# Kernel optimization log

Hardware: AMD Instinct MI355X
Metric: run time of the kernel (lower is better)

## Reference

```python
import jax, jax.numpy as jnp
import numpy as np


def conv1x1(x, w, b):
    # x: [B,C,H,W], w: [O,C], b: [O]
    return jnp.einsum('oc,bchw->bohw', w, x) + b[None, :, None, None]


def interp_bilinear_ac(x, oh, ow):
    # bilinear resize with align_corners=True, x: [B,C,H,W] -> [B,C,oh,ow]
    B, C, H, W = x.shape
    if (H, W) == (oh, ow):
        return x
    ys = jnp.linspace(0.0, H - 1.0, oh)
    xs = jnp.linspace(0.0, W - 1.0, ow)
    y0 = jnp.clip(jnp.floor(ys).astype(jnp.int32), 0, H - 1)
    y1 = jnp.minimum(y0 + 1, H - 1)
    x0 = jnp.clip(jnp.floor(xs).astype(jnp.int32), 0, W - 1)
    x1 = jnp.minimum(x0 + 1, W - 1)
    wy = (ys - y0).astype(x.dtype)
    wx = (xs - x0).astype(x.dtype)
    top = x[:, :, y0, :] * (1 - wy)[None, None, :, None] + x[:, :, y1, :] * wy[None, None, :, None]
    out = top[:, :, :, x0] * (1 - wx)[None, None, None, :] + top[:, :, :, x1] * wx[None, None, None, :]
    return out


def non_local(x, qw, qb, kw, kb, vw, vb, ow_, ob):
    B, C, H, W = x.shape
    HW = H * W
    q = conv1x1(x, qw, qb).reshape(B, -1, HW)  # [B, Ci, HW]
    k = conv1x1(x, kw, kb).reshape(B, -1, HW)
    v = conv1x1(x, vw, vb).reshape(B, -1, HW)
    attn = jnp.einsum('bci,bcj->bij', q, k)     # [B, HW, HW]
    attn = jax.nn.softmax(attn, axis=-1)
    out = jnp.einsum('bcj,bij->bci', v, attn)   # [B, Ci, HW]
    out = out.reshape(B, -1, H, W)
    return conv1x1(out, ow_, ob)


def _forward(x1, x2, x3, x4, qw, qb, kw, kb, vw, vb, ow_, ob, g1w, g1b, g2w, g2b):
    H1, W1 = x1.shape[2], x1.shape[3]
    x2_up = interp_bilinear_ac(x2, H1, W1)
    x3_up = interp_bilinear_ac(x3, H1, W1)
    x4_up = interp_bilinear_ac(x4, H1, W1)
    gf = jnp.concatenate([x1, x2_up, x3_up, x4_up], axis=1)  # [B, 128, H1, W1]
    gf = non_local(gf, qw, qb, kw, kb, vw, vb, ow_, ob)
    h = jax.nn.relu(conv1x1(gf, g1w, g1b))
    sw = jax.nn.sigmoid(conv1x1(h, g2w, g2b))                # [B, 128, H1, W1]
    w1, w2, w3, w4 = sw[:, :32], sw[:, 32:64], sw[:, 64:96], sw[:, 96:128]
    x1_out = x1 * (1 + w1)
    x2_out = x2 * (1 + interp_bilinear_ac(w2, x2.shape[2], x2.shape[3]))
    x3_out = x3 * (1 + interp_bilinear_ac(w3, x3.shape[2], x3.shape[3]))
    x4_out = x4 * (1 + interp_bilinear_ac(w4, x4.shape[2], x4.shape[3]))
    return (x1_out, x2_out, x3_out, x4_out)


def setup_inputs() -> dict:
    key = jax.random.key(0)
    ks = jax.random.split(key, 16)
    C = 128  # channel*4
    Ci = 64  # inter_channel
    Cg = 32
    d = {
        'x1': jax.random.normal(ks[0], (8, 32, 64, 64), jnp.float32),
        'x2': jax.random.normal(ks[1], (8, 32, 32, 32), jnp.float32),
        'x3': jax.random.normal(ks[2], (8, 32, 16, 16), jnp.float32),
        'x4': jax.random.normal(ks[3], (8, 32, 8, 8), jnp.float32),
        'qw': jax.random.normal(ks[4], (Ci, C), jnp.float32) * 0.05,
        'qb': jnp.zeros((Ci,), jnp.float32),
        'kw': jax.random.normal(ks[5], (Ci, C), jnp.float32) * 0.05,
        'kb': jnp.zeros((Ci,), jnp.float32),
        'vw': jax.random.normal(ks[6], (Ci, C), jnp.float32) * 0.05,
        'vb': jnp.zeros((Ci,), jnp.float32),
        'ow_': jax.random.normal(ks[7], (C, Ci), jnp.float32) * 0.05,
        'ob': jnp.zeros((C,), jnp.float32),
        'g1w': jax.random.normal(ks[8], (Cg, C), jnp.float32) * 0.05,
        'g1b': jnp.zeros((Cg,), jnp.float32),
        'g2w': jax.random.normal(ks[9], (C, Cg), jnp.float32) * 0.05,
        'g2b': jnp.zeros((C,), jnp.float32),
    }
    return d


def reference(x1, x2, x3, x4, qw, qb, kw, kb, vw, vb, ow_, ob, g1w, g1b, g2w, g2b):
    return _forward(x1, x2, x3, x4, qw, qb, kw, kb, vw, vb, ow_, ob, g1w, g1b, g2w, g2b)
```

## Files before the change

kernel.cpp:

```cpp
#include <hip/hip_runtime.h>
#include <hip/hip_bf16.h>


typedef __attribute__((ext_vector_type(8))) short s16x8;
typedef __attribute__((ext_vector_type(4))) float f32x4;

#define LOG2E 1.44269504088896340736f

__device__ __forceinline__ unsigned int f2bf(float f) {
    unsigned int u = __float_as_uint(f);
    u += 0x7fffu + ((u >> 16) & 1u);
    return u >> 16;
}
__device__ __forceinline__ unsigned int pk2bf(float a, float b) {
    union { __hip_bfloat162 h; unsigned int u; } cv;
    cv.h = __float22bfloat162_rn(make_float2(a, b));
    return cv.u;
}
__device__ __forceinline__ float bf2f(unsigned short u) {
    return __uint_as_float((unsigned int)u << 16);
}

__global__ __launch_bounds__(256) void k_prep(
    const float* __restrict__ qw, const float* __restrict__ qb,
    const float* __restrict__ kw, const float* __restrict__ kb,
    const float* __restrict__ vw, const float* __restrict__ vb,
    const float* __restrict__ ow, const float* __restrict__ g1w,
    const float* __restrict__ g2w,
    unsigned short* __restrict__ WTb, float* __restrict__ bqkv,
    unsigned short* __restrict__ owb, unsigned short* __restrict__ g1wb,
    unsigned short* __restrict__ g2wb) {
  int t = blockIdx.x * 256 + threadIdx.x;
  if (t < 192 * 128) {
    int oc = t >> 7, c = t & 127;
    float v;
    if (oc < 64)       v = qw[oc * 128 + c] * LOG2E;
    else if (oc < 128) v = kw[(oc - 64) * 128 + c];
    else               v = vw[(oc - 128) * 128 + c];
    WTb[t] = (unsigned short)f2bf(v);
  }
  if (t < 192) {
    float v;
    if (t < 64)       v = qb[t] * LOG2E;
    else if (t < 128) v = kb[t - 64];
    else              v = vb[t - 128];
    bqkv[t] = v;
  }
  if (t < 128 * 64) g1wb[t & 4095] = (unsigned short)f2bf(g1w[t & 4095]);
  if (t < 128 * 64) owb[t] = (unsigned short)f2bf(ow[t]);
  if (t < 128 * 32) g2wb[t] = (unsigned short)f2bf(g2w[t]);
}

__global__ __launch_bounds__(256) void k_qkv(
    const float* __restrict__ x1, const float* __restrict__ x2,
    const float* __restrict__ x3, const float* __restrict__ x4,
    const unsigned short* __restrict__ WTb, const float* __restrict__ bqkv,
    unsigned short* __restrict__ Qg, unsigned short* __restrict__ Kg,
    unsigned short* __restrict__ Vg) {
  __shared__ __align__(16) unsigned short gfb[128 * 136];
  unsigned int* gfbu = (unsigned int*)gfb;

  const int b = blockIdx.x >> 5;
  const int i0 = (blockIdx.x & 31) << 7;
  const int t = threadIdx.x;

  {
    const int cp = t >> 2, q = t & 3;
    const int c0 = cp << 1;
    const int pbase = q << 5;
    const int oy = (i0 >> 6) + (q >> 1);
    const int ox0 = (q & 1) << 5;

    if (cp < 16) {
      const float* s0 = x1 + (((b * 32 + c0) << 12) + (oy << 6) + ox0);
      const float* s1 = s0 + 4096;
      #pragma unroll
      for (int k8 = 0; k8 < 8; k8++) {
        float4 va = ((const float4*)s0)[k8];
        float4 vb = ((const float4*)s1)[k8];
        int p = pbase + k8 * 4;
        gfbu[(p + 0) * 68 + cp] = pk2bf(va.x, vb.x);
        gfbu[(p + 1) * 68 + cp] = pk2bf(va.y, vb.y);
        gfbu[(p + 2) * 68 + cp] = pk2bf(va.z, vb.z);
        gfbu[(p + 3) * 68 + cp] = pk2bf(va.w, vb.w);
      }
    } else {
      const float* base; int S, cs;
      if (cp < 32)      { base = x2; S = 32; cs = c0 - 32; }
      else if (cp < 48) { base = x3; S = 16; cs = c0 - 64; }
      else              { base = x4; S = 8;  cs = c0 - 96; }
      const float* pl0 = base + (b * 32 + cs) * S * S;
      const float* pl1 = pl0 + S * S;
      float yf = (float)oy * (float)(S - 1) * (1.0f / 63.0f);
      int y0 = (int)yf; if (y0 > S - 1) y0 = S - 1;
      int y1 = y0 + 1;  if (y1 > S - 1) y1 = S - 1;
      float wy = yf - (float)y0;
      const float* r00 = pl0 + y0 * S; const float* r01 = pl0 + y1 * S;
      const float* r10 = pl1 + y0 * S; const float* r11 = pl1 + y1 * S;
      for (int k = 0; k < 32; k++) {
        int ox = ox0 + k;
        float xf = (float)ox * (float)(S - 1) * (1.0f / 63.0f);
        int xx0 = (int)xf; if (xx0 > S - 1) xx0 = S - 1;
        int xx1 = xx0 + 1; if (xx1 > S - 1) xx1 = S - 1;
        float wx = xf - (float)xx0;
        float a0 = r00[xx0] + wx * (r00[xx1] - r00[xx0]);
        float b0 = r01[xx0] + wx * (r01[xx1] - r01[xx0]);
        float v0 = a0 + wy * (b0 - a0);
        float a1 = r10[xx0] + wx * (r10[xx1] - r10[xx0]);
        float b1 = r11[xx0] + wx * (r11[xx1] - r11[xx0]);
        float v1 = a1 + wy * (b1 - a1);
        gfbu[(pbase + k) * 68 + cp] = pk2bf(v0, v1);
      }
    }
  }
  __syncthreads();

  const int wv = t >> 6, lane = t & 63;
  const int r = lane & 15, qd = lane >> 4;
  const int ocb = wv * 48;

  s16x8 af[3][4];
  #pragma unroll
  for (int mti = 0; mti < 3; mti++)
    #pragma unroll
    for (int ks = 0; ks < 4; ks++)
      af[mti][ks] = *(const s16x8*)&WTb[(ocb + mti * 16 + r) * 128 + ks * 32 + qd * 8];
  float4 bias[3];
  #pragma unroll
  for (int mti = 0; mti < 3; mti++)
    bias[mti] = *(const float4*)&bqkv[ocb + mti * 16 + qd * 4];

  f32x4 zf = {0.f, 0.f, 0.f, 0.f};
  #pragma unroll 1
  for (int nt = 0; nt < 8; nt++) {
    s16x8 bfr[4];
    #pragma unroll
    for (int ks = 0; ks < 4; ks++)
      bfr[ks] = *(const s16x8*)&gfb[(nt * 16 + r) * 136 + ks * 32 + qd * 8];
    f32x4 acc[3] = {zf, zf, zf};
    #pragma unroll
    for (int ks = 0; ks < 4; ks++)
      #pragma unroll
      for (int mti = 0; mti < 3; mti++)
        acc[mti] = __builtin_amdgcn_mfma_f32_16x16x32_bf16(af[mti][ks], bfr[ks], acc[mti], 0, 0, 0);

    const int pos = i0 + nt * 16 + r;
    #pragma unroll
    for (int mti = 0; mti < 3; mti++) {
      const int gmt = wv * 3 + mti;
      float ax = acc[mti].x + bias[mti].x;
      float ay = acc[mti].y + bias[mti].y;
      float az = acc[mti].z + bias[mti].z;
      float aw = acc[mti].w + bias[mti].w;
      if (gmt < 4) {
        uint2 w; w.x = pk2bf(ax, ay); w.y = pk2bf(az, aw);
        *(uint2*)&Qg[(((b << 12) + pos) << 6) + gmt * 16 + qd * 4] = w;
      } else if (gmt < 8) {
        uint2 w; w.x = pk2bf(ax, ay); w.y = pk2bf(az, aw);
        *(uint2*)&Kg[(((b << 12) + pos) << 6) + (gmt - 4) * 16 + qd * 4] = w;
      } else {
        int ocv = (gmt - 8) * 16 + qd * 4;
        Vg[((b * 64 + ocv + 0) << 12) + pos] = (unsigned short)f2bf(ax);
        Vg[((b * 64 + ocv + 1) << 12) + pos] = (unsigned short)f2bf(ay);
        Vg[((b * 64 + ocv + 2) << 12) + pos] = (unsigned short)f2bf(az);
        Vg[((b * 64 + ocv + 3) << 12) + pos] = (unsigned short)f2bf(aw);
      }
    }
  }
}

__global__ __launch_bounds__(256, 4) void k_attn(
    const unsigned short* __restrict__ Qg, const unsigned short* __restrict__ Kg,
    const unsigned short* __restrict__ Vg, unsigned short* __restrict__ Op,
    float* __restrict__ Lp) {
  __shared__ __align__(16) unsigned short Kl[64 * 72];
  __shared__ __align__(16) unsigned short Vl[64 * 72];
  __shared__ __align__(16) unsigned short Pl[4][32 * 72];

  const int b = blockIdx.x >> 7;
  const int part = (blockIdx.x >> 5) & 3;
  const int qg = blockIdx.x & 31;
  const int i0 = qg << 7;
  const int t = threadIdx.x;
  const int wv = t >> 6, lane = t & 63;
  const int r = lane & 15, qd = lane >> 4;
  const int qbase = i0 + wv * 32;

  s16x8 qf[2][2];
  #pragma unroll
  for (int nt = 0; nt < 2; nt++)
    #pragma unroll
    for (int ks = 0; ks < 2; ks++)
      qf[nt][ks] = *(const s16x8*)&Qg[(((b << 12) + qbase + nt * 16 + r) << 6) + ks * 32 + qd * 8];

  f32x4 zf = {0.f, 0.f, 0.f, 0.f};
  f32x4 acc[2][4];
  #pragma unroll
  for (int nt = 0; nt < 2; nt++)
    #pragma unroll
    for (int mt = 0; mt < 4; mt++) acc[nt][mt] = zf;
  float l[2] = {0.f, 0.f};

  const int srow = t >> 3, sseg = t & 7;
  const unsigned short* kt0 = &Kg[(((b << 12) + (part << 10) + srow) << 6) + sseg * 8];
  const unsigned short* vt0 = &Vg[((b * 64 + srow) << 12) + (part << 10) + sseg * 8];
  uint4 pk0 = *(const uint4*)(kt0);
  uint4 pk1 = *(const uint4*)(kt0 + (32 << 6));
  uint4 pv0 = *(const uint4*)(vt0);
  uint4 pv1 = *(const uint4*)(vt0 + (32 << 12));

  for (int it = 0; it < 16; it++) {
    __syncthreads();
    *(uint4*)&Kl[srow * 72 + sseg * 8] = pk0;
    *(uint4*)&Kl[(srow + 32) * 72 + sseg * 8] = pk1;
    *(uint4*)&Vl[srow * 72 + sseg * 8] = pv0;
    *(uint4*)&Vl[(srow + 32) * 72 + sseg * 8] = pv1;
    __syncthreads();
    if (it < 15) {
      int j0 = (it + 1) << 6;
      pk0 = *(const uint4*)(kt0 + (j0 << 6));
      pk1 = *(const uint4*)(kt0 + ((j0 + 32) << 6));
      pv0 = *(const uint4*)(vt0 + j0);
      pv1 = *(const uint4*)(vt0 + (32 << 12) + j0);
    }

    f32x4 st[4][2];
    #pragma unroll
    for (int mt = 0; mt < 4; mt++) {
      s16x8 kf0 = *(const s16x8*)&Kl[(mt * 16 + r) * 72 + qd * 8];
      s16x8 kf1 = *(const s16x8*)&Kl[(mt * 16 + r) * 72 + 32 + qd * 8];
      #pragma unroll
      for (int nt = 0; nt < 2; nt++) {
        f32x4 s = __builtin_amdgcn_mfma_f32_16x16x32_bf16(kf0, qf[nt][0], zf, 0, 0, 0);
        s = __builtin_amdgcn_mfma_f32_16x16x32_bf16(kf1, qf[nt][1], s, 0, 0, 0);
        st[mt][nt] = s;
      }
    }

    #pragma unroll
    for (int nt = 0; nt < 2; nt++) {
      float rs = 0.f;
      #pragma unroll
      for (int mt = 0; mt < 4; mt++) {
        float px = exp2f(fminf(st[mt][nt].x, 80.f));
        float py = exp2f(fminf(st[mt][nt].y, 80.f));
        float pz = exp2f(fminf(st[mt][nt].z, 80.f));
        float pw = exp2f(fminf(st[mt][nt].w, 80.f));
        rs += (px + py) + (pz + pw);
        uint2 w;
        w.x = pk2bf(px, py);
        w.y = pk2bf(pz, pw);
        *(uint2*)&Pl[wv][(nt * 16 + r) * 72 + mt * 16 + qd * 4] = w;
      }
      rs += __shfl_xor(rs, 16);
      rs += __shfl_xor(rs, 32);
      l[nt] += rs;
    }
    __builtin_amdgcn_wave_barrier();

    #pragma unroll
    for (int ks = 0; ks < 2; ks++) {
      s16x8 pf0 = *(const s16x8*)&Pl[wv][(r) * 72 + ks * 32 + qd * 8];
      s16x8 pf1 = *(const s16x8*)&Pl[wv][(16 + r) * 72 + ks * 32 + qd * 8];
      #pragma unroll
      for (int mt = 0; mt < 4; mt++) {
        s16x8 vf = *(const s16x8*)&Vl[(mt * 16 + r) * 72 + ks * 32 + qd * 8];
        acc[0][mt] = __builtin_amdgcn_mfma_f32_16x16x32_bf16(vf, pf0, acc[0][mt], 0, 0, 0);
        acc[1][mt] = __builtin_amdgcn_mfma_f32_16x16x32_bf16(vf, pf1, acc[1][mt], 0, 0, 0);
      }
    }
  }

  #pragma unroll
  for (int nt = 0; nt < 2; nt++) {
    float inv = 1.0f / l[nt];
    int qrow = qbase + nt * 16 + r;
    unsigned short* orow = &Op[(((part * 8 + b) << 12) + qrow) << 6];
    #pragma unroll
    for (int mt = 0; mt < 4; mt++) {
      uint2 w;
      w.x = pk2bf(acc[nt][mt].x * inv, acc[nt][mt].y * inv);
      w.y = pk2bf(acc[nt][mt].z * inv, acc[nt][mt].w * inv);
      *(uint2*)&orow[mt * 16 + qd * 4] = w;
    }
    if (qd == 0) Lp[((part * 8 + b) << 12) + qrow] = l[nt];
  }
}

__global__ __launch_bounds__(256) void k_out(
    const unsigned short* __restrict__ Op, const float* __restrict__ Lp,
    const unsigned short* __restrict__ owb, const float* __restrict__ obias,
    const unsigned short* __restrict__ g1wb, const float* __restrict__ g1b,
    const unsigned short* __restrict__ g2wb, const float* __restrict__ g2b,
    unsigned short* __restrict__ SWb) {
  __shared__ __align__(16) unsigned short Ot[128 * 72];
  __shared__ __align__(16) unsigned short gf2t[128 * 136];
  __shared__ __align__(16) unsigned short ht[128 * 40];
  const int b = blockIdx.x >> 5;
  const int i0 = (blockIdx.x & 31) << 7;
  const int t = threadIdx.x;

  {
    const int pos = t >> 1, half = t & 1;
    const int i = i0 + pos;
    float lp4[4], lsum = 0.f;
    #pragma unroll
    for (int p = 0; p < 4; p++) { lp4[p] = Lp[((p * 8 + b) << 12) + i]; lsum += lp4[p]; }
    float o[32];
    #pragma unroll
    for (int k = 0; k < 32; k++) o[k] = 0.f;
    #pragma unroll
    for (int p = 0; p < 4; p++) {
      float w = lp4[p] / lsum;
      const uint2* prow = (const uint2*)&Op[((((p * 8 + b) << 12) + i) << 6) + half * 32];
      #pragma unroll
      for (int k = 0; k < 8; k++) {
        uint2 u = prow[k];
        o[k * 4 + 0] += w * __uint_as_float(u.x << 16);
        o[k * 4 + 1] += w * __uint_as_float(u.x & 0xFFFF0000u);
        o[k * 4 + 2] += w * __uint_as_float(u.y << 16);
        o[k * 4 + 3] += w * __uint_as_float(u.y & 0xFFFF0000u);
      }
    }
    unsigned int* dst = (unsigned int*)&Ot[pos * 72 + half * 32];
    #pragma unroll
    for (int k = 0; k < 16; k++) dst[k] = pk2bf(o[2 * k], o[2 * k + 1]);
  }
  __syncthreads();

  const int wv = t >> 6, lane = t & 63;
  const int r = lane & 15, qd = lane >> 4;
  f32x4 zf = {0.f, 0.f, 0.f, 0.f};

  {
    const int ocb = wv * 32;
    s16x8 af[2][2];
    #pragma unroll
    for (int mt = 0; mt < 2; mt++)
      #pragma unroll
      for (int ks = 0; ks < 2; ks++)
        af[mt][ks] = *(const s16x8*)&owb[(ocb + mt * 16 + r) * 64 + ks * 32 + qd * 8];
    float4 bias[2];
    #pragma unroll
    for (int mt = 0; mt < 2; mt++)
      bias[mt] = *(const float4*)&obias[ocb + mt * 16 + qd * 4];
    #pragma unroll 1
    for (int nt = 0; nt < 8; nt++) {
      s16x8 bfr[2];
      #pragma unroll
      for (int ks = 0; ks < 2; ks++)
        bfr[ks] = *(const s16x8*)&Ot[(nt * 16 + r) * 72 + ks * 32 + qd * 8];
      f32x4 acc[2] = {zf, zf};
      #pragma unroll
      for (int ks = 0; ks < 2; ks++)
        #pragma unroll
        for (int mt = 0; mt < 2; mt++)
          acc[mt] = __builtin_amdgcn_mfma_f32_16x16x32_bf16(af[mt][ks], bfr[ks], acc[mt], 0, 0, 0);
      #pragma unroll
      for (int mt = 0; mt < 2; mt++) {
        uint2 w;
        w.x = pk2bf(acc[mt].x + bias[mt].x, acc[mt].y + bias[mt].y);
        w.y = pk2bf(acc[mt].z + bias[mt].z, acc[mt].w + bias[mt].w);
        *(uint2*)&gf2t[(nt * 16 + r) * 136 + ocb + mt * 16 + qd * 4] = w;
      }
    }
  }
  __syncthreads();

  {
    s16x8 af[2][4];
    #pragma unroll
    for (int mt = 0; mt < 2; mt++)
      #pragma unroll
      for (int ks = 0; ks < 4; ks++)
        af[mt][ks] = *(const s16x8*)&g1wb[(mt * 16 + r) * 128 + ks * 32 + qd * 8];
    float4 bias[2];
    #pragma unroll
    for (int mt = 0; mt < 2; mt++)
      bias[mt] = *(const float4*)&g1b[mt * 16 + qd * 4];
    #pragma unroll
    for (int nt = 0; nt < 2; nt++) {
      const int pn = (wv * 2 + nt) * 16 + r;
      s16x8 bfr[4];
      #pragma unroll
      for (int ks = 0; ks < 4; ks++)
        bfr[ks] = *(const s16x8*)&gf2t[pn * 136 + ks * 32 + qd * 8];
      f32x4 acc[2] = {zf, zf};
      #pragma unroll
      for (int ks = 0; ks < 4; ks++)
        #pragma unroll
        for (int mt = 0; mt < 2; mt++)
          acc[mt] = __builtin_amdgcn_mfma_f32_16x16x32_bf16(af[mt][ks], bfr[ks], acc[mt], 0, 0, 0);
      #pragma unroll
      for (int mt = 0; mt < 2; mt++) {
        uint2 w;
        w.x = pk2bf(fmaxf(acc[mt].x + bias[mt].x, 0.f), fmaxf(acc[mt].y + bias[mt].y, 0.f));
        w.y = pk2bf(fmaxf(acc[mt].z + bias[mt].z, 0.f), fmaxf(acc[mt].w + bias[mt].w, 0.f));
        *(uint2*)&ht[pn * 40 + mt * 16 + qd * 4] = w;
      }
    }
  }
  __syncthreads();

  {
    const int nb = wv * 32;
    s16x8 bfg[2];
    float bias[2];
    #pragma unroll
    for (int ntl = 0; ntl < 2; ntl++) {
      bfg[ntl] = *(const s16x8*)&g2wb[(nb + ntl * 16 + r) * 32 + qd * 8];
      bias[ntl] = g2b[nb + ntl * 16 + r];
    }
    #pragma unroll 1
    for (int mt = 0; mt < 8; mt++) {
      s16x8 af = *(const s16x8*)&ht[(mt * 16 + r) * 40 + qd * 8];
      #pragma unroll
      for (int ntl = 0; ntl < 2; ntl++) {
        f32x4 acc = __builtin_amdgcn_mfma_f32_16x16x32_bf16(af, bfg[ntl], zf, 0, 0, 0);
        const int oc3 = nb + ntl * 16 + r;
        float s0 = 1.0f / (1.0f + exp2f(-LOG2E * (acc.x + bias[ntl])));
        float s1 = 1.0f / (1.0f + exp2f(-LOG2E * (acc.y + bias[ntl])));
        float s2 = 1.0f / (1.0f + exp2f(-LOG2E * (acc.z + bias[ntl])));
        float s3 = 1.0f / (1.0f + exp2f(-LOG2E * (acc.w + bias[ntl])));
        uint2 w; w.x = pk2bf(s0, s1); w.y = pk2bf(s2, s3);
        *(uint2*)&SWb[((b * 128 + oc3) << 12) + i0 + mt * 16 + qd * 4] = w;
      }
    }
  }
}

__device__ __forceinline__ float bilin64(const unsigned short* __restrict__ p,
                                         int oy, int ox, int n) {
  float yf = (float)oy * 63.0f / (float)n;
  int y0 = (int)yf; if (y0 > 63) y0 = 63;
  int y1 = y0 + 1;  if (y1 > 63) y1 = 63;
  float wy = yf - (float)y0;
  float xf = (float)ox * 63.0f / (float)n;
  int x0 = (int)xf; if (x0 > 63) x0 = 63;
  int x1 = x0 + 1;  if (x1 > 63) x1 = 63;
  float wx = xf - (float)x0;
  float v00 = bf2f(p[y0 * 64 + x0]), v01 = bf2f(p[y0 * 64 + x1]);
  float v10 = bf2f(p[y1 * 64 + x0]), v11 = bf2f(p[y1 * 64 + x1]);
  float top = v00 + wx * (v01 - v00);
  float bot = v10 + wx * (v11 - v10);
  return top + wy * (bot - top);
}

__global__ __launch_bounds__(256) void k_final(
    const float* __restrict__ x1, const float* __restrict__ x2,
    const float* __restrict__ x3, const float* __restrict__ x4,
    const unsigned short* __restrict__ SWb, float* __restrict__ out) {
  const int N1 = 1048576, N2 = 262144, N3 = 65536, N4 = 16384;
  int idx = blockIdx.x * 256 + threadIdx.x;
  if (idx < N1) {
    int b = idx >> 17, rr = idx & 131071;
    int c = rr >> 12, hw = rr & 4095;
    out[idx] = x1[idx] * (1.f + bf2f(SWb[((b * 128 + c) << 12) + hw]));
  } else if (idx < N1 + N2) {
    int i2 = idx - N1;
    int b = i2 >> 15, rr = i2 & 32767;
    int c = rr >> 10, oy = (rr >> 5) & 31, ox = rr & 31;
    float w = bilin64(SWb + ((b * 128 + 32 + c) << 12), oy, ox, 31);
    out[idx] = x2[i2] * (1.f + w);
  } else if (idx < N1 + N2 + N3) {
    int i3 = idx - N1 - N2;
    int b = i3 >> 13, rr = i3 & 8191;
    int c = rr >> 8, oy = (rr >> 4) & 15, ox = rr & 15;
    float w = bilin64(SWb + ((b * 128 + 64 + c) << 12), oy, ox, 15);
    out[idx] = x3[i3] * (1.f + w);
  } else if (idx < N1 + N2 + N3 + N4) {
    int i4 = idx - N1 - N2 - N3;
    int b = i4 >> 11, rr = i4 & 2047;
    int c = rr >> 6, oy = (rr >> 3) & 7, ox = rr & 7;
    float w = bilin64(SWb + ((b * 128 + 96 + c) << 12), oy, ox, 7);
    out[idx] = x4[i4] * (1.f + w);
  }
}

extern "C" void kernel_launch(void* const* d_in, const int* in_sizes, int n_in,
                              void* d_out, int out_size, void* d_ws, size_t ws_size,
                              hipStream_t stream) {
  const float* x1  = (const float*)d_in[0];
  const float* x2  = (const float*)d_in[1];
  const float* x3  = (const float*)d_in[2];
  const float* x4  = (const float*)d_in[3];
  const float* qw  = (const float*)d_in[4];
  const float* qb  = (const float*)d_in[5];
  const float* kw  = (const float*)d_in[6];
  const float* kb  = (const float*)d_in[7];
  const float* vw  = (const float*)d_in[8];
  const float* vb  = (const float*)d_in[9];
  const float* ow  = (const float*)d_in[10];
  const float* ob  = (const float*)d_in[11];
  const float* g1w = (const float*)d_in[12];
  const float* g1b = (const float*)d_in[13];
  const float* g2w = (const float*)d_in[14];
  const float* g2b = (const float*)d_in[15];
  float* out = (float*)d_out;

  char* ws = (char*)d_ws;
  unsigned short* Qg  = (unsigned short*)(ws + 0);
  unsigned short* Kg  = (unsigned short*)(ws + 4194304);
  unsigned short* Vg  = (unsigned short*)(ws + 8388608);
  unsigned short* SWb = (unsigned short*)(ws + 0);
  unsigned short* Op  = (unsigned short*)(ws + 12582912);
  float* Lp   = (float*)(ws + 29360128);
  unsigned short* WTb = (unsigned short*)(ws + 29884416);
  float* bqkv = (float*)(ws + 29933568);
  unsigned short* owb  = (unsigned short*)(ws + 29934592);
  unsigned short* g1wb = (unsigned short*)(ws + 29950976);
  unsigned short* g2wb = (unsigned short*)(ws + 29959168);

  k_prep<<<96, 256, 0, stream>>>(qw, qb, kw, kb, vw, vb, ow, g1w, g2w,
                                 WTb, bqkv, owb, g1wb, g2wb);
  k_qkv<<<256, 256, 0, stream>>>(x1, x2, x3, x4, WTb, bqkv, Qg, Kg, Vg);
  k_attn<<<1024, 256, 0, stream>>>(Qg, Kg, Vg, Op, Lp);
  k_out<<<256, 256, 0, stream>>>(Op, Lp, owb, ob, g1wb, g1b, g2wb, g2b, SWb);
  k_final<<<5440, 256, 0, stream>>>(x1, x2, x3, x4, SWb, out);
}
```

Before: 201.7 us.

## Compute softmax row sums via MFMA, use fast exp2/rcp, and split qkv tiles

The attention kernel no longer accumulates row sums with per-element adds and cross-lane shuffles. It gets them from an extra MFMA against a ones vector, which also lets exp be fused right after the QK MFMA without a staging array. exp2f and divisions are replaced with hardware exp2/rcp intrinsics in attention, merge and sigmoid, at slightly lower accuracy. k_qkv now processes 64 positions per block with twice as many blocks, halving shared memory to raise occupancy and parallelism.

```diff
diff --git a/kernel.cpp b/kernel.cpp
--- a/kernel.cpp
+++ b/kernel.cpp
@@ -19,6 +19,12 @@
 }
 __device__ __forceinline__ float bf2f(unsigned short u) {
     return __uint_as_float((unsigned int)u << 16);
+}
+__device__ __forceinline__ float fexp2(float x) {
+    return __builtin_amdgcn_exp2f(x);
+}
+__device__ __forceinline__ float frcp(float x) {
+    return __builtin_amdgcn_rcpf(x);
 }
 
 __global__ __launch_bounds__(256) void k_prep(
@@ -57,28 +63,28 @@
     const unsigned short* __restrict__ WTb, const float* __restrict__ bqkv,
     unsigned short* __restrict__ Qg, unsigned short* __restrict__ Kg,
     unsigned short* __restrict__ Vg) {
-  __shared__ __align__(16) unsigned short gfb[128 * 136];
+  __shared__ __align__(16) unsigned short gfb[64 * 136];
   unsigned int* gfbu = (unsigned int*)gfb;
 
-  const int b = blockIdx.x >> 5;
-  const int i0 = (blockIdx.x & 31) << 7;
+  const int b = blockIdx.x >> 6;
+  const int i0 = (blockIdx.x & 63) << 6;
   const int t = threadIdx.x;
 
   {
     const int cp = t >> 2, q = t & 3;
     const int c0 = cp << 1;
-    const int pbase = q << 5;
-    const int oy = (i0 >> 6) + (q >> 1);
-    const int ox0 = (q & 1) << 5;
+    const int pbase = q << 4;
+    const int oy = i0 >> 6;
+    const int ox0 = pbase;
 
     if (cp < 16) {
       const float* s0 = x1 + (((b * 32 + c0) << 12) + (oy << 6) + ox0);
       const float* s1 = s0 + 4096;
       #pragma unroll
-      for (int k8 = 0; k8 < 8; k8++) {
-        float4 va = ((const float4*)s0)[k8];
-        float4 vb = ((const float4*)s1)[k8];
-        int p = pbase + k8 * 4;
+      for (int k4 = 0; k4 < 4; k4++) {
+        float4 va = ((const float4*)s0)[k4];
+        float4 vb = ((const float4*)s1)[k4];
+        int p = pbase + k4 * 4;
         gfbu[(p + 0) * 68 + cp] = pk2bf(va.x, vb.x);
         gfbu[(p + 1) * 68 + cp] = pk2bf(va.y, vb.y);
         gfbu[(p + 2) * 68 + cp] = pk2bf(va.z, vb.z);
@@ -97,7 +103,7 @@
       float wy = yf - (float)y0;
       const float* r00 = pl0 + y0 * S; const float* r01 = pl0 + y1 * S;
       const float* r10 = pl1 + y0 * S; const float* r11 = pl1 + y1 * S;
-      for (int k = 0; k < 32; k++) {
+      for (int k = 0; k < 16; k++) {
         int ox = ox0 + k;
         float xf = (float)ox * (float)(S - 1) * (1.0f / 63.0f);
         int xx0 = (int)xf; if (xx0 > S - 1) xx0 = S - 1;
@@ -132,7 +138,7 @@
 
   f32x4 zf = {0.f, 0.f, 0.f, 0.f};
   #pragma unroll 1
-  for (int nt = 0; nt < 8; nt++) {
+  for (int nt = 0; nt < 4; nt++) {
     s16x8 bfr[4];
     #pragma unroll
     for (int ks = 0; ks < 4; ks++)
@@ -199,7 +205,10 @@
   for (int nt = 0; nt < 2; nt++)
     #pragma unroll
     for (int mt = 0; mt < 4; mt++) acc[nt][mt] = zf;
-  float l[2] = {0.f, 0.f};
+  f32x4 accl[2] = {zf, zf};
+
+  const short ob = (r == 0) ? (short)0x3F80 : (short)0;
+  const s16x8 vones = {ob, ob, ob, ob, ob, ob, ob, ob};
 
   const int srow = t >> 3, sseg = t & 7;
   const unsigned short* kt0 = &Kg[(((b << 12) + (part << 10) + srow) << 6) + sseg * 8];
@@ -224,7 +233,6 @@
       pv1 = *(const uint4*)(vt0 + (32 << 12) + j0);
     }
 
-    f32x4 st[4][2];
     #pragma unroll
     for (int mt = 0; mt < 4; mt++) {
       s16x8 kf0 = *(const s16x8*)&Kl[(mt * 16 + r) * 72 + qd * 8];
@@ -233,28 +241,15 @@
       for (int nt = 0; nt < 2; nt++) {
         f32x4 s = __builtin_amdgcn_mfma_f32_16x16x32_bf16(kf0, qf[nt][0], zf, 0, 0, 0);
         s = __builtin_amdgcn_mfma_f32_16x16x32_bf16(kf1, qf[nt][1], s, 0, 0, 0);
-        st[mt][nt] = s;
-      }
-    }
-
-    #pragma unroll
-    for (int nt = 0; nt < 2; nt++) {
-      float rs = 0.f;
-      #pragma unroll
-      for (int mt = 0; mt < 4; mt++) {
-        float px = exp2f(fminf(st[mt][nt].x, 80.f));
-        float py = exp2f(fminf(st[mt][nt].y, 80.f));
-        float pz = exp2f(fminf(st[mt][nt].z, 80.f));
-        float pw = exp2f(fminf(st[mt][nt].w, 80.f));
-        rs += (px + py) + (pz + pw);
+        float px = fexp2(fminf(s.x, 80.f));
+        float py = fexp2(fminf(s.y, 80.f));
+        float pz = fexp2(fminf(s.z, 80.f));
+        float pw = fexp2(fminf(s.w, 80.f));
         uint2 w;
         w.x = pk2bf(px, py);
         w.y = pk2bf(pz, pw);
         *(uint2*)&Pl[wv][(nt * 16 + r) * 72 + mt * 16 + qd * 4] = w;
       }
-      rs += __shfl_xor(rs, 16);
-      rs += __shfl_xor(rs, 32);
-      l[nt] += rs;
     }
     __builtin_amdgcn_wave_barrier();
 
@@ -268,12 +263,15 @@
         acc[0][mt] = __builtin_amdgcn_mfma_f32_16x16x32_bf16(vf, pf0, acc[0][mt], 0, 0, 0);
         acc[1][mt] = __builtin_amdgcn_mfma_f32_16x16x32_bf16(vf, pf1, acc[1][mt], 0, 0, 0);
       }
+      accl[0] = __builtin_amdgcn_mfma_f32_16x16x32_bf16(vones, pf0, accl[0], 0, 0, 0);
+      accl[1] = __builtin_amdgcn_mfma_f32_16x16x32_bf16(vones, pf1, accl[1], 0, 0, 0);
     }
   }
 
   #pragma unroll
   for (int nt = 0; nt < 2; nt++) {
-    float inv = 1.0f / l[nt];
+    float lv = __shfl(accl[nt].x, r);
+    float inv = frcp(lv);
     int qrow = qbase + nt * 16 + r;
     unsigned short* orow = &Op[(((part * 8 + b) << 12) + qrow) << 6];
     #pragma unroll
@@ -283,7 +281,7 @@
       w.y = pk2bf(acc[nt][mt].z * inv, acc[nt][mt].w * inv);
       *(uint2*)&orow[mt * 16 + qd * 4] = w;
     }
-    if (qd == 0) Lp[((part * 8 + b) << 12) + qrow] = l[nt];
+    if (qd == 0) Lp[((part * 8 + b) << 12) + qrow] = lv;
   }
 }
 
@@ -309,9 +307,10 @@
     float o[32];
     #pragma unroll
     for (int k = 0; k < 32; k++) o[k] = 0.f;
+    float invs = frcp(lsum);
     #pragma unroll
     for (int p = 0; p < 4; p++) {
-      float w = lp4[p] / lsum;
+      float w = lp4[p] * invs;
       const uint2* prow = (const uint2*)&Op[((((p * 8 + b) << 12) + i) << 6) + half * 32];
       #pragma unroll
       for (int k = 0; k < 8; k++) {
@@ -418,10 +417,10 @@
       for (int ntl = 0; ntl < 2; ntl++) {
         f32x4 acc = __builtin_amdgcn_mfma_f32_16x16x32_bf16(af, bfg[ntl], zf, 0, 0, 0);
         const int oc3 = nb + ntl * 16 + r;
-        float s0 = 1.0f / (1.0f + exp2f(-LOG2E * (acc.x + bias[ntl])));
-        float s1 = 1.0f / (1.0f + exp2f(-LOG2E * (acc.y + bias[ntl])));
-        float s2 = 1.0f / (1.0f + exp2f(-LOG2E * (acc.z + bias[ntl])));
-        float s3 = 1.0f / (1.0f + exp2f(-LOG2E * (acc.w + bias[ntl])));
+        float s0 = frcp(1.0f + fexp2(-LOG2E * (acc.x + bias[ntl])));
+        float s1 = frcp(1.0f + fexp2(-LOG2E * (acc.y + bias[ntl])));
+        float s2 = frcp(1.0f + fexp2(-LOG2E * (acc.z + bias[ntl])));
+        float s3 = frcp(1.0f + fexp2(-LOG2E * (acc.w + bias[ntl])));
         uint2 w; w.x = pk2bf(s0, s1); w.y = pk2bf(s2, s3);
         *(uint2*)&SWb[((b * 128 + oc3) << 12) + i0 + mt * 16 + qd * 4] = w;
       }
@@ -513,7 +512,7 @@
 
   k_prep<<<96, 256, 0, stream>>>(qw, qb, kw, kb, vw, vb, ow, g1w, g2w,
                                  WTb, bqkv, owb, g1wb, g2wb);
-  k_qkv<<<256, 256, 0, stream>>>(x1, x2, x3, x4, WTb, bqkv, Qg, Kg, Vg);
+  k_qkv<<<512, 256, 0, stream>>>(x1, x2, x3, x4, WTb, bqkv, Qg, Kg, Vg);
   k_attn<<<1024, 256, 0, stream>>>(Qg, Kg, Vg, Op, Lp);
   k_out<<<256, 256, 0, stream>>>(Op, Lp, owb, ob, g1wb, g1b, g2wb, g2b, SWb);
   k_final<<<5440, 256, 0, stream>>>(x1, x2, x3, x4, SWb, out);
```

Result: faster. 184.4 us (-8.6%).
